# Optimization experiments

Hardware: AMD Instinct MI355X
Metric: run time of the kernel (lower is better)

The kernel has to match this reference:

```python
import jax, jax.numpy as jnp
import numpy as np
from math import tan, atan

N = 4_000_000
W_PX, H_PX = 1920, 1080
ZNEAR, ZFAR = 0.1, 100.0
FOVX = 1.0471975512  # 60 deg
FOVY = 2.0 * atan(tan(0.5 * FOVX) * H_PX / W_PX)
RELAX = 1.3


def _projection_matrix():
    # Camera.get_projection_matrix with left=-right, bottom=-top (offsets vanish)
    right = ZNEAR * tan(0.5 * FOVX)
    top = ZNEAR * tan(0.5 * FOVY)
    return np.array([
        [ZNEAR / right, 0.0, 0.0, 0.0],
        [0.0, ZNEAR / top, 0.0, 0.0],
        [0.0, 0.0, ZFAR / (ZFAR - ZNEAR), -ZFAR * ZNEAR / (ZFAR - ZNEAR)],
        [0.0, 0.0, 1.0, 0.0],
    ], dtype=np.float32)


def setup_inputs() -> dict:
    key = jax.random.key(0)
    k1, k2, k3 = jax.random.split(key, 3)
    # positions: xy spread in front of camera, z strictly positive (in-frustum-ish)
    xy = jax.random.uniform(k1, (N, 2), minval=-6.0, maxval=6.0, dtype=jnp.float32)
    z = jax.random.uniform(k2, (N, 1), minval=0.5, maxval=30.0, dtype=jnp.float32)
    pos3d = jnp.concatenate([xy, z], axis=1)  # (N,3)
    # symmetric PSD 3x3 covariances
    A = jax.random.normal(k3, (N, 3, 3), dtype=jnp.float32) * 0.1
    cov3d = A @ A.swapaxes(-1, -2)  # (N,3,3)
    view_matrix = jnp.eye(4, dtype=jnp.float32)  # world2model (camera at origin)
    projection_matrix = jnp.asarray(_projection_matrix())
    return {"pos3d": pos3d, "cov3d": cov3d,
            "view_matrix": view_matrix, "projection_matrix": projection_matrix}


def reference(pos3d, cov3d, view_matrix, projection_matrix):
    # --- project position with MVP (pos3d @ view.T then @ proj.T) ---
    Vt = view_matrix.T
    p_model = pos3d @ Vt[:3, :3] + Vt[3, :3]                       # (N,3)
    ones = jnp.ones((p_model.shape[0], 1), dtype=p_model.dtype)
    p_h = jnp.concatenate([p_model, ones], axis=1)                 # (N,4)
    p_clip = p_h @ projection_matrix.T                             # (N,4)
    p_ndc = p_clip[:, :3] / (p_clip[:, 3:4] + 1e-6)                # (N,3)

    # --- view-frustum cull mask ---
    mask = ((p_ndc[:, 2] >= 0.2)
            & (p_ndc[:, 0] >= -RELAX) & (p_ndc[:, 0] <= RELAX)
            & (p_ndc[:, 1] >= -RELAX) & (p_ndc[:, 1] <= RELAX))

    # --- screen-space position (masked; original gathers pos[mask], we keep full-N padded) ---
    sx = 0.5 * (p_ndc[:, 0] + 1.0) * W_PX
    sy = (1.0 - 0.5 * (p_ndc[:, 1] + 1.0)) * H_PX
    pos2d = jnp.where(mask[:, None], jnp.stack([sx, sy, p_ndc[:, 2]], axis=1), 0.0)

    # --- 2D covariance: J @ W @ cov3d @ W.T @ J.T ---
    Wm = view_matrix[:3, :3].T                                     # (3,3)
    x, y, z = pos3d[:, 0], pos3d[:, 1], pos3d[:, 2]
    inv_z = 1.0 / z
    zeros = jnp.zeros_like(z)
    J = jnp.stack([
        jnp.stack([inv_z, zeros, -x * inv_z], axis=1),
        jnp.stack([zeros, inv_z, -y * inv_z], axis=1),
    ], axis=1)                                                     # (N,2,3)
    M = jnp.einsum('ij,njk,lk->nil', Wm, cov3d, Wm)                # (N,3,3)
    cov2d = jnp.einsum('nij,njk,nlk->nil', J, M, J)                # (N,2,2)
    cov2d = jnp.where(mask[:, None, None], cov2d, 0.0)
    return pos2d, cov2d, mask
```

## Files before the change

kernel.cpp:

```cpp
#include <hip/hip_runtime.h>

#define PXW 1920.0f
#define PXH 1080.0f
#define RELAXF 1.3f

#define NT 256
#define TILE_PTS 1024
#define POS_F4 768
#define COV_F4 2304

typedef float f4 __attribute__((ext_vector_type(4)));

__device__ __forceinline__ int swz(int s) { return s ^ ((s >> 3) & 7); }

__global__ __launch_bounds__(NT, 3) void cam_kernel(
    const float* __restrict__ pos3d,
    const float* __restrict__ cov3d,
    const float* __restrict__ view,
    const float* __restrict__ proj,
    float* __restrict__ out,
    int n)
{
  __shared__ f4 sPos[POS_F4];
  __shared__ f4 sCov[COV_F4];

  const int b = blockIdx.x;
  const int t = threadIdx.x;
  const long long p0 = (long long)b * TILE_PTS;

  float V[12];
  float P[16];
#pragma unroll
  for (int i = 0; i < 12; ++i) V[i] = view[i];
#pragma unroll
  for (int i = 0; i < 16; ++i) P[i] = proj[i];

  if (p0 + TILE_PTS <= n) {
    const f4* gp = reinterpret_cast<const f4*>(pos3d) + (size_t)POS_F4 * b;
    const f4* gc = reinterpret_cast<const f4*>(cov3d) + (size_t)COV_F4 * b;
    f4 rp[3], rc[9];
#pragma unroll
    for (int j = 0; j < 3; ++j) rp[j] = gp[t + NT * j];
#pragma unroll
    for (int j = 0; j < 9; ++j) rc[j] = gc[t + NT * j];
#pragma unroll
    for (int j = 0; j < 3; ++j) sPos[t + NT * j] = rp[j];
#pragma unroll
    for (int j = 0; j < 9; ++j) sCov[swz(t + NT * j)] = rc[j];
    __syncthreads();

    const f4 pa = sPos[3 * t + 0];
    const f4 pb = sPos[3 * t + 1];
    const f4 pc = sPos[3 * t + 2];
    float cf[36];
#pragma unroll
    for (int j = 0; j < 9; ++j) {
      const f4 c = sCov[swz(9 * t + j)];
      cf[4 * j + 0] = c.x; cf[4 * j + 1] = c.y;
      cf[4 * j + 2] = c.z; cf[4 * j + 3] = c.w;
    }

    float px[4], py[4], pz[4];
    px[0] = pa.x; py[0] = pa.y; pz[0] = pa.z;
    px[1] = pa.w; py[1] = pb.x; pz[1] = pb.y;
    px[2] = pb.z; py[2] = pb.w; pz[2] = pc.x;
    px[3] = pc.y; py[3] = pc.z; pz[3] = pc.w;

    float o_pos[12], o_cov[16], o_msk[4];

#pragma unroll
    for (int k = 0; k < 4; ++k) {
      const float x = px[k], y = py[k], z = pz[k];

      const float pm0 = V[0] * x + V[1] * y + V[2]  * z + V[3];
      const float pm1 = V[4] * x + V[5] * y + V[6]  * z + V[7];
      const float pm2 = V[8] * x + V[9] * y + V[10] * z + V[11];

      const float c0 = P[0]  * pm0 + P[1]  * pm1 + P[2]  * pm2 + P[3];
      const float c1 = P[4]  * pm0 + P[5]  * pm1 + P[6]  * pm2 + P[7];
      const float c2 = P[8]  * pm0 + P[9]  * pm1 + P[10] * pm2 + P[11];
      const float c3 = P[12] * pm0 + P[13] * pm1 + P[14] * pm2 + P[15];

      const float iw = 1.0f / (c3 + 1e-6f);
      const float nx = c0 * iw, ny = c1 * iw, nz = c2 * iw;

      const bool m = (nz >= 0.2f) && (nx >= -RELAXF) && (nx <= RELAXF)
                                  && (ny >= -RELAXF) && (ny <= RELAXF);

      const float sx = 0.5f * (nx + 1.0f) * PXW;
      const float sy = (1.0f - 0.5f * (ny + 1.0f)) * PXH;

      o_pos[3 * k + 0] = m ? sx : 0.0f;
      o_pos[3 * k + 1] = m ? sy : 0.0f;
      o_pos[3 * k + 2] = m ? nz : 0.0f;
      o_msk[k]         = m ? 1.0f : 0.0f;

      const float iz = 1.0f / z;
      const float a0 = iz * (V[0] - x * V[2]);
      const float a1 = iz * (V[4] - x * V[6]);
      const float a2 = iz * (V[8] - x * V[10]);
      const float b0 = iz * (V[1] - y * V[2]);
      const float b1 = iz * (V[5] - y * V[6]);
      const float b2 = iz * (V[9] - y * V[10]);

      const float* C = &cf[9 * k];
      const float u0 = C[0] * a0 + C[1] * a1 + C[2] * a2;
      const float u1 = C[3] * a0 + C[4] * a1 + C[5] * a2;
      const float u2 = C[6] * a0 + C[7] * a1 + C[8] * a2;
      const float v0 = C[0] * b0 + C[1] * b1 + C[2] * b2;
      const float v1 = C[3] * b0 + C[4] * b1 + C[5] * b2;
      const float v2 = C[6] * b0 + C[7] * b1 + C[8] * b2;

      o_cov[4 * k + 0] = m ? (a0 * u0 + a1 * u1 + a2 * u2) : 0.0f;
      o_cov[4 * k + 1] = m ? (a0 * v0 + a1 * v1 + a2 * v2) : 0.0f;
      o_cov[4 * k + 2] = m ? (b0 * u0 + b1 * u1 + b2 * u2) : 0.0f;
      o_cov[4 * k + 3] = m ? (b0 * v0 + b1 * v1 + b2 * v2) : 0.0f;
    }

    f4 tm = { o_msk[0], o_msk[1], o_msk[2], o_msk[3] };
    reinterpret_cast<f4*>(out + (size_t)7 * n)[(size_t)NT * b + t] = tm;

    __syncthreads();
#pragma unroll
    for (int c = 0; c < 3; ++c) {
      f4 v = { o_pos[4 * c + 0], o_pos[4 * c + 1],
               o_pos[4 * c + 2], o_pos[4 * c + 3] };
      sCov[swz(3 * t + c)] = v;
    }
#pragma unroll
    for (int c = 0; c < 4; ++c) {
      f4 v = { o_cov[4 * c + 0], o_cov[4 * c + 1],
               o_cov[4 * c + 2], o_cov[4 * c + 3] };
      sCov[swz(POS_F4 + 4 * t + c)] = v;
    }
    __syncthreads();

    f4* opg = reinterpret_cast<f4*>(out) + (size_t)POS_F4 * b;
#pragma unroll
    for (int j = 0; j < 3; ++j) opg[t + NT * j] = sCov[swz(t + NT * j)];

    f4* ocg = reinterpret_cast<f4*>(out + (size_t)3 * n) + (size_t)1024 * b;
#pragma unroll
    for (int j = 0; j < 4; ++j)
      ocg[t + NT * j] = sCov[swz(POS_F4 + t + NT * j)];

  } else {
    for (long long g = p0 / 4 + t; 4 * g < n; g += NT) {
      const float4* p4 = reinterpret_cast<const float4*>(pos3d) + (size_t)3 * g;
      const float4 pa = p4[0], pb = p4[1], pc = p4[2];
      float px[4], py[4], pz[4];
      px[0] = pa.x; py[0] = pa.y; pz[0] = pa.z;
      px[1] = pa.w; py[1] = pb.x; pz[1] = pb.y;
      px[2] = pb.z; py[2] = pb.w; pz[2] = pc.x;
      px[3] = pc.y; py[3] = pc.z; pz[3] = pc.w;

      const float4* c4 = reinterpret_cast<const float4*>(cov3d) + (size_t)9 * g;
      float cf[36];
#pragma unroll
      for (int i = 0; i < 9; ++i) {
        const float4 tt = c4[i];
        cf[4 * i + 0] = tt.x; cf[4 * i + 1] = tt.y;
        cf[4 * i + 2] = tt.z; cf[4 * i + 3] = tt.w;
      }

      float o_pos[12], o_cov[16], o_msk[4];
#pragma unroll
      for (int k = 0; k < 4; ++k) {
        const float x = px[k], y = py[k], z = pz[k];
        const float pm0 = V[0] * x + V[1] * y + V[2]  * z + V[3];
        const float pm1 = V[4] * x + V[5] * y + V[6]  * z + V[7];
        const float pm2 = V[8] * x + V[9] * y + V[10] * z + V[11];
        const float c0 = P[0]  * pm0 + P[1]  * pm1 + P[2]  * pm2 + P[3];
        const float c1 = P[4]  * pm0 + P[5]  * pm1 + P[6]  * pm2 + P[7];
        const float c2 = P[8]  * pm0 + P[9]  * pm1 + P[10] * pm2 + P[11];
        const float c3 = P[12] * pm0 + P[13] * pm1 + P[14] * pm2 + P[15];
        const float iw = 1.0f / (c3 + 1e-6f);
        const float nx = c0 * iw, ny = c1 * iw, nz = c2 * iw;
        const bool m = (nz >= 0.2f) && (nx >= -RELAXF) && (nx <= RELAXF)
                                    && (ny >= -RELAXF) && (ny <= RELAXF);
        const float sx = 0.5f * (nx + 1.0f) * PXW;
        const float sy = (1.0f - 0.5f * (ny + 1.0f)) * PXH;
        o_pos[3 * k + 0] = m ? sx : 0.0f;
        o_pos[3 * k + 1] = m ? sy : 0.0f;
        o_pos[3 * k + 2] = m ? nz : 0.0f;
        o_msk[k]         = m ? 1.0f : 0.0f;
        const float iz = 1.0f / z;
        const float a0 = iz * (V[0] - x * V[2]);
        const float a1 = iz * (V[4] - x * V[6]);
        const float a2 = iz * (V[8] - x * V[10]);
        const float b0 = iz * (V[1] - y * V[2]);
        const float b1 = iz * (V[5] - y * V[6]);
        const float b2 = iz * (V[9] - y * V[10]);
        const float* C = &cf[9 * k];
        const float u0 = C[0] * a0 + C[1] * a1 + C[2] * a2;
        const float u1 = C[3] * a0 + C[4] * a1 + C[5] * a2;
        const float u2 = C[6] * a0 + C[7] * a1 + C[8] * a2;
        const float v0 = C[0] * b0 + C[1] * b1 + C[2] * b2;
        const float v1 = C[3] * b0 + C[4] * b1 + C[5] * b2;
        const float v2 = C[6] * b0 + C[7] * b1 + C[8] * b2;
        o_cov[4 * k + 0] = m ? (a0 * u0 + a1 * u1 + a2 * u2) : 0.0f;
        o_cov[4 * k + 1] = m ? (a0 * v0 + a1 * v1 + a2 * v2) : 0.0f;
        o_cov[4 * k + 2] = m ? (b0 * u0 + b1 * u1 + b2 * u2) : 0.0f;
        o_cov[4 * k + 3] = m ? (b0 * v0 + b1 * v1 + b2 * v2) : 0.0f;
      }

      float4* op = reinterpret_cast<float4*>(out) + (size_t)3 * g;
      op[0] = make_float4(o_pos[0], o_pos[1], o_pos[2],  o_pos[3]);
      op[1] = make_float4(o_pos[4], o_pos[5], o_pos[6],  o_pos[7]);
      op[2] = make_float4(o_pos[8], o_pos[9], o_pos[10], o_pos[11]);
      float4* oc = reinterpret_cast<float4*>(out + (size_t)3 * n) + (size_t)4 * g;
#pragma unroll
      for (int k = 0; k < 4; ++k)
        oc[k] = make_float4(o_cov[4 * k + 0], o_cov[4 * k + 1],
                            o_cov[4 * k + 2], o_cov[4 * k + 3]);
      reinterpret_cast<float4*>(out + (size_t)7 * n)[g] =
          make_float4(o_msk[0], o_msk[1], o_msk[2], o_msk[3]);
    }
  }
}

extern "C" void kernel_launch(void* const* d_in, const int* in_sizes, int n_in,
                              void* d_out, int out_size, void* d_ws, size_t ws_size,
                              hipStream_t stream) {
  const float* pos3d = (const float*)d_in[0];
  const float* cov3d = (const float*)d_in[1];
  const float* view  = (const float*)d_in[2];
  const float* proj  = (const float*)d_in[3];

  const int n = in_sizes[0] / 3;

  const int blocks = (n + TILE_PTS - 1) / TILE_PTS;
  cam_kernel<<<blocks, NT, 0, stream>>>(pos3d, cov3d, view, proj,
                                        (float*)d_out, n);
}
```

Baseline: 278.8 us.

## Restructure tile staging to per-wavefront slices without block barriers

Each 64-lane wavefront now owns its own 256-point slice and a private LDS region, so the block-wide __syncthreads barriers are removed. Positions are read directly from global memory instead of through LDS, and the swizzle is replaced with a padded stride for the covariance output staging. Occupancy hint rises from 3 to 4 blocks per CU. This relies on wavefront-level lockstep execution for LDS visibility and may bring back LDS bank conflicts where the swizzle used to avoid them.

```diff
diff --git a/kernel.cpp b/kernel.cpp
--- a/kernel.cpp
+++ b/kernel.cpp
@@ -3,17 +3,13 @@
 #define PXW 1920.0f
 #define PXH 1080.0f
 #define RELAXF 1.3f
-
 #define NT 256
-#define TILE_PTS 1024
-#define POS_F4 768
-#define COV_F4 2304
 
 typedef float f4 __attribute__((ext_vector_type(4)));
 
-__device__ __forceinline__ int swz(int s) { return s ^ ((s >> 3) & 7); }
-
-__global__ __launch_bounds__(NT, 3) void cam_kernel(
+#define WSLICE 576
+
+__global__ __launch_bounds__(NT, 4) void cam_kernel(
     const float* __restrict__ pos3d,
     const float* __restrict__ cov3d,
     const float* __restrict__ view,
@@ -21,41 +17,36 @@
     float* __restrict__ out,
     int n)
 {
-  __shared__ f4 sPos[POS_F4];
-  __shared__ f4 sCov[COV_F4];
-
-  const int b = blockIdx.x;
-  const int t = threadIdx.x;
-  const long long p0 = (long long)b * TILE_PTS;
-
-  float V[12];
-  float P[16];
+  __shared__ f4 sBuf[4 * WSLICE];
+
+  const int l   = threadIdx.x & 63;
+  const int w   = threadIdx.x >> 6;
+  const int wt  = blockIdx.x * 4 + w;
+  const int nwt = n >> 8;
+  f4* S = sBuf + w * WSLICE;
+
+  float V[12], P[16];
 #pragma unroll
   for (int i = 0; i < 12; ++i) V[i] = view[i];
 #pragma unroll
   for (int i = 0; i < 16; ++i) P[i] = proj[i];
 
-  if (p0 + TILE_PTS <= n) {
-    const f4* gp = reinterpret_cast<const f4*>(pos3d) + (size_t)POS_F4 * b;
-    const f4* gc = reinterpret_cast<const f4*>(cov3d) + (size_t)COV_F4 * b;
-    f4 rp[3], rc[9];
-#pragma unroll
-    for (int j = 0; j < 3; ++j) rp[j] = gp[t + NT * j];
-#pragma unroll
-    for (int j = 0; j < 9; ++j) rc[j] = gc[t + NT * j];
-#pragma unroll
-    for (int j = 0; j < 3; ++j) sPos[t + NT * j] = rp[j];
-#pragma unroll
-    for (int j = 0; j < 9; ++j) sCov[swz(t + NT * j)] = rc[j];
-    __syncthreads();
-
-    const f4 pa = sPos[3 * t + 0];
-    const f4 pb = sPos[3 * t + 1];
-    const f4 pc = sPos[3 * t + 2];
+  if (wt < nwt) {
+    const f4* gc = reinterpret_cast<const f4*>(cov3d) + (size_t)576 * wt;
+    f4 rc[9];
+#pragma unroll
+    for (int j = 0; j < 9; ++j) rc[j] = gc[l + 64 * j];
+
+    const f4* gp = reinterpret_cast<const f4*>(pos3d) + (size_t)192 * wt + 3 * l;
+    const f4 pa = gp[0], pb = gp[1], pc = gp[2];
+
+#pragma unroll
+    for (int j = 0; j < 9; ++j) S[l + 64 * j] = rc[j];
+
     float cf[36];
 #pragma unroll
     for (int j = 0; j < 9; ++j) {
-      const f4 c = sCov[swz(9 * t + j)];
+      const f4 c = S[9 * l + j];
       cf[4 * j + 0] = c.x; cf[4 * j + 1] = c.y;
       cf[4 * j + 2] = c.z; cf[4 * j + 3] = c.w;
     }
@@ -118,41 +109,41 @@
     }
 
     f4 tm = { o_msk[0], o_msk[1], o_msk[2], o_msk[3] };
-    reinterpret_cast<f4*>(out + (size_t)7 * n)[(size_t)NT * b + t] = tm;
-
-    __syncthreads();
+    reinterpret_cast<f4*>(out + (size_t)7 * n)[(size_t)64 * wt + l] = tm;
+
 #pragma unroll
     for (int c = 0; c < 3; ++c) {
       f4 v = { o_pos[4 * c + 0], o_pos[4 * c + 1],
                o_pos[4 * c + 2], o_pos[4 * c + 3] };
-      sCov[swz(3 * t + c)] = v;
+      S[3 * l + c] = v;
     }
 #pragma unroll
     for (int c = 0; c < 4; ++c) {
       f4 v = { o_cov[4 * c + 0], o_cov[4 * c + 1],
                o_cov[4 * c + 2], o_cov[4 * c + 3] };
-      sCov[swz(POS_F4 + 4 * t + c)] = v;
-    }
-    __syncthreads();
-
-    f4* opg = reinterpret_cast<f4*>(out) + (size_t)POS_F4 * b;
-#pragma unroll
-    for (int j = 0; j < 3; ++j) opg[t + NT * j] = sCov[swz(t + NT * j)];
-
-    f4* ocg = reinterpret_cast<f4*>(out + (size_t)3 * n) + (size_t)1024 * b;
-#pragma unroll
-    for (int j = 0; j < 4; ++j)
-      ocg[t + NT * j] = sCov[swz(POS_F4 + t + NT * j)];
-
-  } else {
-    for (long long g = p0 / 4 + t; 4 * g < n; g += NT) {
+      S[192 + 5 * l + c] = v;
+    }
+
+    f4* gop = reinterpret_cast<f4*>(out) + (size_t)192 * wt;
+#pragma unroll
+    for (int j = 0; j < 3; ++j) gop[l + 64 * j] = S[l + 64 * j];
+
+    f4* goc = reinterpret_cast<f4*>(out + (size_t)3 * n) + (size_t)256 * wt;
+#pragma unroll
+    for (int j = 0; j < 4; ++j) {
+      const int i = l + 64 * j;
+      goc[i] = S[192 + 5 * (i >> 2) + (i & 3)];
+    }
+
+  } else if (wt == nwt) {
+    for (int g = nwt * 64 + l; g < (n >> 2); g += 64) {
       const float4* p4 = reinterpret_cast<const float4*>(pos3d) + (size_t)3 * g;
-      const float4 pa = p4[0], pb = p4[1], pc = p4[2];
+      const float4 ta = p4[0], tb = p4[1], tc = p4[2];
       float px[4], py[4], pz[4];
-      px[0] = pa.x; py[0] = pa.y; pz[0] = pa.z;
-      px[1] = pa.w; py[1] = pb.x; pz[1] = pb.y;
-      px[2] = pb.z; py[2] = pb.w; pz[2] = pc.x;
-      px[3] = pc.y; py[3] = pc.z; pz[3] = pc.w;
+      px[0] = ta.x; py[0] = ta.y; pz[0] = ta.z;
+      px[1] = ta.w; py[1] = tb.x; pz[1] = tb.y;
+      px[2] = tb.z; py[2] = tb.w; pz[2] = tc.x;
+      px[3] = tc.y; py[3] = tc.z; pz[3] = tc.w;
 
       const float4* c4 = reinterpret_cast<const float4*>(cov3d) + (size_t)9 * g;
       float cf[36];
@@ -229,7 +220,8 @@
 
   const int n = in_sizes[0] / 3;
 
-  const int blocks = (n + TILE_PTS - 1) / TILE_PTS;
+  const int groups = n >> 2;
+  const int blocks = (groups + 4 * 64 - 1) / (4 * 64);
   cam_kernel<<<blocks, NT, 0, stream>>>(pos3d, cov3d, view, proj,
                                         (float*)d_out, n);
 }
```

Result: no change. 278.6 us (-0.1%).
